# Kernel tuning notes

Hardware: AMD Instinct MI355X
Metric: run time of the kernel (lower is better)

The kernel has to match this reference:

```python
import jax, jax.numpy as jnp
import numpy as np

D_MODEL = 1024
N_HEADS = 16
D_V = D_MODEL // N_HEADS  # 64


def setup_inputs() -> dict:
    key = jax.random.key(0)
    k1, k2, k3, k4, k5, k6 = jax.random.split(key, 6)
    N, L = 2, 2048
    return {
        "queries": jax.random.normal(k1, (N, L, D_MODEL), jnp.float32),
        "keys": jax.random.normal(k2, (N, L, D_MODEL), jnp.float32),
        "values": jax.random.normal(k3, (N, L, D_MODEL), jnp.float32),
        # key-padding mask, 0 = masked out (broadcast over heads and queries)
        "mask": jax.random.randint(k4, (N, 1, 1, L), 0, 2).astype(jnp.int32),
        # torch nn.Linear(d_model, d_model): weight [out, in], bias [out]
        "fc_w": jax.random.normal(k5, (D_MODEL, D_MODEL), jnp.float32) / np.sqrt(D_MODEL).astype(np.float32),
        "fc_b": jax.random.normal(k6, (D_MODEL,), jnp.float32) * 0.01,
    }


def reference(queries, keys, values, mask, fc_w, fc_b):
    N, Lq, _ = queries.shape
    Lk = keys.shape[1]
    # NOTE: the source defines Q/K/V Linear layers but never applies them in forward.
    q = queries.reshape(N, Lq, N_HEADS, D_V).transpose(0, 2, 1, 3)  # [N,H,Lq,Dv]
    k = keys.reshape(N, Lk, N_HEADS, D_V)                            # [N,Lk,H,Dv]
    v = values.reshape(N, Lk, N_HEADS, D_V)                          # [N,Lk,H,Dv]
    energy = jnp.einsum('nhqd,nkhd->nhqk', q, k)                     # QK^T
    energy = jnp.where(mask == 0, -jnp.inf, energy)                  # masked_fill
    # faithful to source: scale by sqrt(d_model), applied after masking
    attn = jax.nn.softmax(energy / jnp.sqrt(jnp.float32(D_MODEL)), axis=-1)
    out = jnp.einsum('nhqk,nkhd->nqhd', attn, v).reshape(N, Lq, N_HEADS * D_V)
    return out @ fc_w.T + fc_b
```

## Files before the change

kernel.cpp:

```cpp
#include <hip/hip_runtime.h>
#include <hip/hip_bf16.h>

#define SEQL 2048
#define DMODEL 1024

typedef short bf16x8 __attribute__((ext_vector_type(8)));
typedef short bf16x4 __attribute__((ext_vector_type(4)));
typedef float f32x4 __attribute__((ext_vector_type(4)));
typedef unsigned short u16;

__device__ __forceinline__ u16 f2bf(float f) {
    union { float f; unsigned u; } v; v.f = f;
    unsigned r = v.u + 0x7FFFu + ((v.u >> 16) & 1u);
    return (u16)(r >> 16);
}

__device__ __forceinline__ float fexp2(float x) {
#if __has_builtin(__builtin_amdgcn_exp2f)
    return __builtin_amdgcn_exp2f(x);
#else
    return exp2f(x);
#endif
}

#define SCALE2 0.04508422f

__device__ __forceinline__ void async16(u16* lds, const u16* g) {
    __builtin_amdgcn_global_load_lds(
        (const __attribute__((address_space(1))) unsigned int*)g,
        (__attribute__((address_space(3))) unsigned int*)lds,
        16, 0, 0);
}


#define TSTR 72

__global__ __launch_bounds__(256) void pack_all(
    const float* __restrict__ kg, const float* __restrict__ wg,
    const float* __restrict__ vg, const int* __restrict__ mg,
    u16* __restrict__ kb, u16* __restrict__ wb, u16* __restrict__ vtb,
    float* __restrict__ maskf)
{
    __shared__ __align__(16) u16 T[64 * TSTR];
    const int b = blockIdx.x, t = threadIdx.x;
    u16 o[8];
    if (b < 2048) {
        const int e0 = (b * 256 + t) * 8;
        const int n = e0 >> 21;
        const int s = (e0 >> 10) & 2047;
        const int dm = e0 & 1023, h = dm >> 6, d0 = dm & 63;
        const float4 x0 = *(const float4*)(kg + e0);
        const float4 x1 = *(const float4*)(kg + e0 + 4);
        o[0]=f2bf(x0.x); o[1]=f2bf(x0.y); o[2]=f2bf(x0.z); o[3]=f2bf(x0.w);
        o[4]=f2bf(x1.x); o[5]=f2bf(x1.y); o[6]=f2bf(x1.z); o[7]=f2bf(x1.w);
        const int kt = s >> 6, st = (s >> 4) & 3, m = s & 15;
        const int f = d0 >> 5, qd = (d0 >> 3) & 3;
        u16* dst = kb + ((size_t)((n * 16 + h) * 32 + kt)) * 4096
                      + (st * 2 + f) * 512 + (m + 16 * qd) * 8;
        *(bf16x8*)dst = *(bf16x8*)o;
    } else if (b < 2560) {
        const int e0 = ((b - 2048) * 256 + t) * 8;
        const int col = e0 >> 10, k0 = e0 & 1023;
        const float4 x0 = *(const float4*)(wg + e0);
        const float4 x1 = *(const float4*)(wg + e0 + 4);
        o[0]=f2bf(x0.x); o[1]=f2bf(x0.y); o[2]=f2bf(x0.z); o[3]=f2bf(x0.w);
        o[4]=f2bf(x1.x); o[5]=f2bf(x1.y); o[6]=f2bf(x1.z); o[7]=f2bf(x1.w);
        const int cb = col >> 6, cj = (col >> 4) & 3, m = col & 15;
        const int kt = k0 >> 6, f = (k0 >> 5) & 1, qd = (k0 >> 3) & 3;
        u16* dst = wb + ((size_t)((cb * 16 + kt) * 8 + cj * 2 + f)) * 512
                      + (m + 16 * qd) * 8;
        *(bf16x8*)dst = *(bf16x8*)o;
    } else if (b < 3584) {
        const int bb = b - 2560;
        const int kt = bb & 31, h = (bb >> 5) & 15, n = bb >> 9;
        {
            const int s = t >> 2, d0 = (t & 3) * 16;
            const float* src = vg + ((size_t)(n * SEQL + kt * 64 + s) * DMODEL) + h * 64 + d0;
            u16 w16[16];
            #pragma unroll
            for (int j = 0; j < 16; ++j) w16[j] = f2bf(src[j]);
            *(bf16x8*)&T[s * TSTR + d0]     = *(bf16x8*)&w16[0];
            *(bf16x8*)&T[s * TSTR + d0 + 8] = *(bf16x8*)&w16[8];
        }
        __syncthreads();
        {
            const int d = t >> 2, k0 = (t & 3) * 16;
            u16 w16[16];
            #pragma unroll
            for (int j = 0; j < 16; ++j) w16[j] = T[(k0 + j) * TSTR + d];
            const int t4 = d >> 4, dr = d & 15;
            u16* base = vtb + ((size_t)((n * 16 + h) * 32 + kt)) * 4096;
            #pragma unroll
            for (int g = 0; g < 2; ++g) {
                const int key0 = k0 + g * 8;
                const int kk = key0 >> 5, qk = (key0 >> 3) & 3;
                *(bf16x8*)(base + (t4 * 2 + kk) * 512 + (dr + 16 * qk) * 8)
                    = *(bf16x8*)&w16[g * 8];
            }
        }
    } else {
        #pragma unroll
        for (int i = 0; i < 16; ++i) {
            const int idx = t * 16 + i;
            maskf[idx] = mg[idx] ? 0.0f : -1.0e5f;
        }
    }
}

#define OSPLIT 4194304
#define LSPLIT 65536

template<int NSPLIT>
__global__ __launch_bounds__(256) void attn_kernel(
    const float* __restrict__ qg, const u16* __restrict__ kb,
    const u16* __restrict__ vtb, const float* __restrict__ maskf,
    u16* __restrict__ xb, float* __restrict__ opart, float* __restrict__ lpart)
{
    __shared__ __align__(16) u16 SM[24576];
    u16* const K_lds = SM;
    u16* const V_lds = SM + 8192;
    u16* const P_lds = SM + 16384;

    const int blk = blockIdx.x;
    const int qblk = blk & 15;
    const int h = (blk >> 4) & 15;
    const int n = (blk >> 8) & 1;
    const int split = blk >> 9;
    const int tid = threadIdx.x;
    const int wave = tid >> 6, lane = tid & 63;
    const int lrow = lane & 15, quad = lane >> 4;
    const int q0 = qblk * 128;

    const u16* ksrc0 = kb  + ((size_t)(n * 16 + h)) * 131072;
    const u16* vsrc0 = vtb + ((size_t)(n * 16 + h)) * 131072;
    const float* mrow = maskf + n * SEQL;

    const int ktlo = split * (32 / NSPLIT);
    const int kthi = ktlo + (32 / NSPLIT);

    {
        const u16* ks = ksrc0 + (size_t)ktlo * 4096;
        const u16* vs = vsrc0 + (size_t)ktlo * 4096;
        #pragma unroll
        for (int i = 0; i < 2; ++i) {
            const int ch = tid + i * 256;
            async16(&K_lds[ch * 8], ks + ch * 8);
            async16(&V_lds[ch * 8], vs + ch * 8);
        }
    }

    bf16x8 qf[2][2];
    #pragma unroll
    for (int qi = 0; qi < 2; ++qi) {
        const float* qp = qg + ((size_t)(n * SEQL + q0 + wave * 32 + qi * 16 + lrow) * DMODEL) + h * 64 + quad * 8;
        #pragma unroll
        for (int f = 0; f < 2; ++f) {
            const float4 a = *(const float4*)(qp + f * 32);
            const float4 c = *(const float4*)(qp + f * 32 + 4);
            u16* dst = (u16*)&qf[qi][f];
            dst[0]=f2bf(a.x); dst[1]=f2bf(a.y); dst[2]=f2bf(a.z); dst[3]=f2bf(a.w);
            dst[4]=f2bf(c.x); dst[5]=f2bf(c.y); dst[6]=f2bf(c.z); dst[7]=f2bf(c.w);
        }
    }

    bf16x8 onesf;
    #pragma unroll
    for (int j = 0; j < 8; ++j) ((u16*)&onesf)[j] = 0x3F80;

    f32x4 oacc[2][4];
    f32x4 lacc[2];
    #pragma unroll
    for (int qi = 0; qi < 2; ++qi) {
        lacc[qi] = (f32x4){0.f, 0.f, 0.f, 0.f};
        #pragma unroll
        for (int t4 = 0; t4 < 4; ++t4) oacc[qi][t4] = (f32x4){0.f, 0.f, 0.f, 0.f};
    }

    __syncthreads();

    for (int kt = ktlo; kt < kthi; ++kt) {
        const int cur = (kt - ktlo) & 1;
        const u16* const Kc = K_lds + cur * 4096;
        const u16* const Vc = V_lds + cur * 4096;

        if (kt + 1 < kthi) {
            const int nxt = cur ^ 1;
            const u16* ks = ksrc0 + (size_t)(kt + 1) * 4096;
            const u16* vs = vsrc0 + (size_t)(kt + 1) * 4096;
            #pragma unroll
            for (int i = 0; i < 2; ++i) {
                const int ch = tid + i * 256;
                async16(&K_lds[nxt * 4096 + ch * 8], ks + ch * 8);
                async16(&V_lds[nxt * 4096 + ch * 8], vs + ch * 8);
            }
        }

        #pragma unroll
        for (int st = 0; st < 4; ++st) {
            const bf16x8 kf0 = *(const bf16x8*)&Kc[(st * 2 + 0) * 512 + lane * 8];
            const bf16x8 kf1 = *(const bf16x8*)&Kc[(st * 2 + 1) * 512 + lane * 8];
            const f32x4 mv = *(const f32x4*)&mrow[kt * 64 + st * 16 + quad * 4];
            const int kk = st >> 1;
            const int qk = (st & 1) * 2 + (quad >> 1);
            const int j0 = (quad & 1) * 4;
            #pragma unroll
            for (int qi = 0; qi < 2; ++qi) {
                f32x4 sa = (f32x4){0.f, 0.f, 0.f, 0.f};
                sa = __builtin_amdgcn_mfma_f32_16x16x32_bf16(kf0, qf[qi][0], sa, 0, 0, 0);
                sa = __builtin_amdgcn_mfma_f32_16x16x32_bf16(kf1, qf[qi][1], sa, 0, 0, 0);
                float e0v = fexp2(fmaf(sa[0], SCALE2, mv[0]));
                float e1v = fexp2(fmaf(sa[1], SCALE2, mv[1]));
                float e2v = fexp2(fmaf(sa[2], SCALE2, mv[2]));
                float e3v = fexp2(fmaf(sa[3], SCALE2, mv[3]));
                __hip_bfloat162 h0 = __float22bfloat162_rn(make_float2(e0v, e1v));
                __hip_bfloat162 h1 = __float22bfloat162_rn(make_float2(e2v, e3v));
                union { unsigned u[2]; bf16x4 v; } pk;
                pk.u[0] = *(unsigned*)&h0;
                pk.u[1] = *(unsigned*)&h1;
                *(bf16x4*)&P_lds[wave * 2048 + (qi * 2 + kk) * 512 + (lrow + 16 * qk) * 8 + j0] = pk.v;
            }
        }
        asm volatile("s_waitcnt lgkmcnt(0)" ::: "memory");

        bf16x8 vf[4][2];
        #pragma unroll
        for (int t4 = 0; t4 < 4; ++t4) {
            vf[t4][0] = *(const bf16x8*)&Vc[(t4 * 2 + 0) * 512 + lane * 8];
            vf[t4][1] = *(const bf16x8*)&Vc[(t4 * 2 + 1) * 512 + lane * 8];
        }
        #pragma unroll
        for (int qi = 0; qi < 2; ++qi) {
            const bf16x8 pf0 = *(const bf16x8*)&P_lds[wave * 2048 + (qi * 2 + 0) * 512 + lane * 8];
            const bf16x8 pf1 = *(const bf16x8*)&P_lds[wave * 2048 + (qi * 2 + 1) * 512 + lane * 8];
            lacc[qi] = __builtin_amdgcn_mfma_f32_16x16x32_bf16(pf0, onesf, lacc[qi], 0, 0, 0);
            lacc[qi] = __builtin_amdgcn_mfma_f32_16x16x32_bf16(pf1, onesf, lacc[qi], 0, 0, 0);
            #pragma unroll
            for (int t4 = 0; t4 < 4; ++t4) {
                oacc[qi][t4] = __builtin_amdgcn_mfma_f32_16x16x32_bf16(pf0, vf[t4][0], oacc[qi][t4], 0, 0, 0);
                oacc[qi][t4] = __builtin_amdgcn_mfma_f32_16x16x32_bf16(pf1, vf[t4][1], oacc[qi][t4], 0, 0, 0);
            }
        }

        __syncthreads();
    }

    if (NSPLIT == 1) {
        #pragma unroll
        for (int qi = 0; qi < 2; ++qi)
            #pragma unroll
            for (int r = 0; r < 4; ++r) {
                const float rinv = 1.0f / lacc[qi][r];
                const int row = n * SEQL + q0 + wave * 32 + qi * 16 + quad * 4 + r;
                const int rb = row >> 7, rt = (row >> 4) & 7, m = row & 15;
                #pragma unroll
                for (int t4 = 0; t4 < 4; ++t4) {
                    const int f = t4 >> 1;
                    const int qd = (t4 & 1) * 2 + (lrow >> 3);
                    xb[((size_t)((rb * 16 + h) * 16 + rt * 2 + f)) * 512
                       + (m + 16 * qd) * 8 + (lrow & 7)] = f2bf(oacc[qi][t4][r] * rinv);
                }
            }
    } else {
        #pragma unroll
        for (int qi = 0; qi < 2; ++qi) {
            #pragma unroll
            for (int r = 0; r < 4; ++r) {
                const int q = q0 + wave * 32 + qi * 16 + quad * 4 + r;
                float* op = opart + (size_t)split * OSPLIT + (size_t)(n * SEQL + q) * DMODEL + h * 64 + lrow;
                #pragma unroll
                for (int t4 = 0; t4 < 4; ++t4)
                    op[t4 * 16] = oacc[qi][t4][r];
                if (lrow == 0)
                    lpart[split * LSPLIT + (n * SEQL + q) * 16 + h] = lacc[qi][r];
            }
        }
    }
}

template<int NSPLIT>
__global__ __launch_bounds__(256) void reduce_norm(
    const float* __restrict__ opart, const float* __restrict__ lpart,
    u16* __restrict__ xb)
{
    const int gid = blockIdx.x * 256 + threadIdx.x;
    const int e0 = gid * 8;
    const int row = e0 >> 10, k0 = e0 & 1023, h = k0 >> 6;
    float lsum = 0.f;
    #pragma unroll
    for (int s = 0; s < NSPLIT; ++s) lsum += lpart[s * LSPLIT + row * 16 + h];
    const float rinv = 1.0f / lsum;
    float a[8] = {0.f,0.f,0.f,0.f,0.f,0.f,0.f,0.f};
    #pragma unroll
    for (int s = 0; s < NSPLIT; ++s) {
        const float4 x0 = *(const float4*)(opart + (size_t)s * OSPLIT + e0);
        const float4 x1 = *(const float4*)(opart + (size_t)s * OSPLIT + e0 + 4);
        a[0]+=x0.x; a[1]+=x0.y; a[2]+=x0.z; a[3]+=x0.w;
        a[4]+=x1.x; a[5]+=x1.y; a[6]+=x1.z; a[7]+=x1.w;
    }
    u16 o[8];
    #pragma unroll
    for (int j = 0; j < 8; ++j) o[j] = f2bf(a[j] * rinv);
    const int rb = row >> 7, rt = (row >> 4) & 7, m = row & 15;
    const int kt = k0 >> 6, f = (k0 >> 5) & 1, qd = (k0 >> 3) & 3;
    *(bf16x8*)(xb + ((size_t)((rb * 16 + kt) * 16 + rt * 2 + f)) * 512
                  + (m + 16 * qd) * 8) = *(bf16x8*)o;
}

__global__ __launch_bounds__(256) void fc_kernel(
    const u16* __restrict__ xb, const u16* __restrict__ wb,
    const float* __restrict__ bias, float* __restrict__ out)
{
    __shared__ __align__(16) u16 SM[24576];
    u16* const X_lds = SM;
    u16* const W_lds = SM + 16384;

    const int blk = blockIdx.x;
    const int cb = blk & 15, rb = blk >> 4;
    const int tid = threadIdx.x;
    const int wave = tid >> 6, lane = tid & 63;
    const int lrow = lane & 15, quad = lane >> 4;

    const u16* xs0 = xb + ((size_t)rb * 16) * 8192;
    const u16* ws0 = wb + ((size_t)cb * 16) * 4096;

    f32x4 acc[2][4];
    #pragma unroll
    for (int ri = 0; ri < 2; ++ri)
        #pragma unroll
        for (int cj = 0; cj < 4; ++cj) acc[ri][cj] = (f32x4){0.f, 0.f, 0.f, 0.f};

    {
        #pragma unroll
        for (int i = 0; i < 4; ++i) {
            const int ch = tid + i * 256;
            async16(&X_lds[ch * 8], xs0 + ch * 8);
        }
        #pragma unroll
        for (int i = 0; i < 2; ++i) {
            const int ch = tid + i * 256;
            async16(&W_lds[ch * 8], ws0 + ch * 8);
        }
    }
    __syncthreads();

    for (int kt = 0; kt < 16; ++kt) {
        const int cur = kt & 1;
        const u16* const Xc = X_lds + cur * 8192;
        const u16* const Wc = W_lds + cur * 4096;

        if (kt + 1 < 16) {
            const int nxt = cur ^ 1;
            const u16* xs = xs0 + (size_t)(kt + 1) * 8192;
            const u16* ws = ws0 + (size_t)(kt + 1) * 4096;
            #pragma unroll
            for (int i = 0; i < 4; ++i) {
                const int ch = tid + i * 256;
                async16(&X_lds[nxt * 8192 + ch * 8], xs + ch * 8);
            }
            #pragma unroll
            for (int i = 0; i < 2; ++i) {
                const int ch = tid + i * 256;
                async16(&W_lds[nxt * 4096 + ch * 8], ws + ch * 8);
            }
        }

        bf16x8 af[2][2];
        #pragma unroll
        for (int ri = 0; ri < 2; ++ri) {
            af[ri][0] = *(const bf16x8*)&Xc[((wave * 2 + ri) * 2 + 0) * 512 + lane * 8];
            af[ri][1] = *(const bf16x8*)&Xc[((wave * 2 + ri) * 2 + 1) * 512 + lane * 8];
        }
        #pragma unroll
        for (int cj = 0; cj < 4; ++cj) {
            const bf16x8 bf0 = *(const bf16x8*)&Wc[(cj * 2 + 0) * 512 + lane * 8];
            const bf16x8 bf1 = *(const bf16x8*)&Wc[(cj * 2 + 1) * 512 + lane * 8];
            #pragma unroll
            for (int ri = 0; ri < 2; ++ri) {
                acc[ri][cj] = __builtin_amdgcn_mfma_f32_16x16x32_bf16(af[ri][0], bf0, acc[ri][cj], 0, 0, 0);
                acc[ri][cj] = __builtin_amdgcn_mfma_f32_16x16x32_bf16(af[ri][1], bf1, acc[ri][cj], 0, 0, 0);
            }
        }

        __syncthreads();
    }

    const int row0 = rb * 128, col0 = cb * 64;
    #pragma unroll
    for (int ri = 0; ri < 2; ++ri)
        #pragma unroll
        for (int cj = 0; cj < 4; ++cj) {
            const int col = col0 + cj * 16 + lrow;
            const float bv = bias[col];
            #pragma unroll
            for (int r = 0; r < 4; ++r)
                out[(size_t)(row0 + wave * 32 + ri * 16 + quad * 4 + r) * DMODEL + col] = acc[ri][cj][r] + bv;
        }
}

extern "C" void kernel_launch(void* const* d_in, const int* in_sizes, int n_in,
                              void* d_out, int out_size, void* d_ws, size_t ws_size,
                              hipStream_t stream) {
    const float* q   = (const float*)d_in[0];
    const float* k   = (const float*)d_in[1];
    const float* v   = (const float*)d_in[2];
    const int*   m   = (const int*)d_in[3];
    const float* fcw = (const float*)d_in[4];
    const float* fcb = (const float*)d_in[5];
    float* out = (float*)d_out;

    char* ws = (char*)d_ws;
    u16*   kbuf  = (u16*)(ws);
    u16*   vtbuf = (u16*)(ws + (8u  << 20));
    u16*   wbuf  = (u16*)(ws + (16u << 20));
    u16*   xbuf  = (u16*)(ws + (18u << 20));
    float* maskf = (float*)(ws + (26u << 20));
    float* opart = (float*)(ws + (27u << 20));
    float* lpart = (float*)(ws + (59u << 20));
    const bool split2 = ws_size >= (60u << 20);

    pack_all<<<dim3(3585), dim3(256), 0, stream>>>(k, fcw, v, m, kbuf, wbuf, vtbuf, maskf);
    if (split2) {
        attn_kernel<2><<<dim3(1024), dim3(256), 0, stream>>>(q, kbuf, vtbuf, maskf, xbuf, opart, lpart);
        reduce_norm<2><<<dim3(2048), dim3(256), 0, stream>>>(opart, lpart, xbuf);
    } else {
        attn_kernel<1><<<dim3(512), dim3(256), 0, stream>>>(q, kbuf, vtbuf, maskf, xbuf, opart, lpart);
    }
    fc_kernel<<<dim3(512), dim3(256), 0, stream>>>(xbuf, wbuf, fcb, out);
}
```

Before: 182.1 us.

## Switch attention to 32x32x16 MFMA with register-resident P via permlane swaps

Rewrites the attention inner loop to use 32x32x16 bf16 MFMAs, computing S as K·Q so that the exponentiated probabilities can be rearranged in registers with v_permlane32_swap and fed straight into the PV MFMA. This removes the P round-trip through LDS and the extra ones-vector MFMAs used for row sums, which are now accumulated in VALU. The K and V^T packing layouts change to match the new fragment shapes, and s_setprio is added around the MFMA bursts. The cost is higher register pressure from 16-wide accumulators and a dependence on the permlane32 swap instruction being available on this target.

```diff
diff --git a/kernel.cpp b/kernel.cpp
--- a/kernel.cpp
+++ b/kernel.cpp
@@ -7,6 +7,7 @@
 typedef short bf16x8 __attribute__((ext_vector_type(8)));
 typedef short bf16x4 __attribute__((ext_vector_type(4)));
 typedef float f32x4 __attribute__((ext_vector_type(4)));
+typedef float f32x16 __attribute__((ext_vector_type(16)));
 typedef unsigned short u16;
 
 __device__ __forceinline__ u16 f2bf(float f) {
@@ -24,6 +25,15 @@
 }
 
 #define SCALE2 0.04508422f
+
+__device__ __forceinline__ unsigned pkbf(float lo, float hi_) {
+    __hip_bfloat162 hh = __float22bfloat162_rn(make_float2(lo, hi_));
+    return *(unsigned*)&hh;
+}
+
+__device__ __forceinline__ void plswap(unsigned &a, unsigned &b) {
+    asm volatile("v_permlane32_swap_b32 %0, %1" : "+v"(a), "+v"(b));
+}
 
 __device__ __forceinline__ void async16(u16* lds, const u16* g) {
     __builtin_amdgcn_global_load_lds(
@@ -53,10 +63,10 @@
         const float4 x1 = *(const float4*)(kg + e0 + 4);
         o[0]=f2bf(x0.x); o[1]=f2bf(x0.y); o[2]=f2bf(x0.z); o[3]=f2bf(x0.w);
         o[4]=f2bf(x1.x); o[5]=f2bf(x1.y); o[6]=f2bf(x1.z); o[7]=f2bf(x1.w);
-        const int kt = s >> 6, st = (s >> 4) & 3, m = s & 15;
-        const int f = d0 >> 5, qd = (d0 >> 3) & 3;
+        const int kt = s >> 6, key = s & 63, kh = key >> 5, m = key & 31;
+        const int f = d0 >> 4, h2 = (d0 >> 3) & 1;
         u16* dst = kb + ((size_t)((n * 16 + h) * 32 + kt)) * 4096
-                      + (st * 2 + f) * 512 + (m + 16 * qd) * 8;
+                      + (kh * 4 + f) * 512 + (m + 32 * h2) * 8;
         *(bf16x8*)dst = *(bf16x8*)o;
     } else if (b < 2560) {
         const int e0 = ((b - 2048) * 256 + t) * 8;
@@ -88,15 +98,12 @@
             u16 w16[16];
             #pragma unroll
             for (int j = 0; j < 16; ++j) w16[j] = T[(k0 + j) * TSTR + d];
-            const int t4 = d >> 4, dr = d & 15;
-            u16* base = vtb + ((size_t)((n * 16 + h) * 32 + kt)) * 4096;
-            #pragma unroll
-            for (int g = 0; g < 2; ++g) {
-                const int key0 = k0 + g * 8;
-                const int kk = key0 >> 5, qk = (key0 >> 3) & 3;
-                *(bf16x8*)(base + (t4 * 2 + kk) * 512 + (dr + 16 * qk) * 8)
-                    = *(bf16x8*)&w16[g * 8];
-            }
+            const int kgp = t & 3;
+            const int dh = d >> 5, m = d & 31;
+            u16* base = vtb + ((size_t)((n * 16 + h) * 32 + kt)) * 4096
+                            + (kgp * 2 + dh) * 512;
+            *(bf16x8*)(base + m * 8)        = *(bf16x8*)&w16[0];
+            *(bf16x8*)(base + (m + 32) * 8) = *(bf16x8*)&w16[8];
         }
     } else {
         #pragma unroll
@@ -116,10 +123,10 @@
     const u16* __restrict__ vtb, const float* __restrict__ maskf,
     u16* __restrict__ xb, float* __restrict__ opart, float* __restrict__ lpart)
 {
-    __shared__ __align__(16) u16 SM[24576];
+    __shared__ __align__(16) u16 SM[16640];
     u16* const K_lds = SM;
     u16* const V_lds = SM + 8192;
-    u16* const P_lds = SM + 16384;
+    float* const LS  = (float*)(SM + 16384);
 
     const int blk = blockIdx.x;
     const int qblk = blk & 15;
@@ -128,7 +135,7 @@
     const int split = blk >> 9;
     const int tid = threadIdx.x;
     const int wave = tid >> 6, lane = tid & 63;
-    const int lrow = lane & 15, quad = lane >> 4;
+    const int l31 = lane & 31, hi = lane >> 5;
     const int q0 = qblk * 128;
 
     const u16* ksrc0 = kb  + ((size_t)(n * 16 + h)) * 131072;
@@ -149,32 +156,26 @@
         }
     }
 
-    bf16x8 qf[2][2];
-    #pragma unroll
-    for (int qi = 0; qi < 2; ++qi) {
-        const float* qp = qg + ((size_t)(n * SEQL + q0 + wave * 32 + qi * 16 + lrow) * DMODEL) + h * 64 + quad * 8;
-        #pragma unroll
-        for (int f = 0; f < 2; ++f) {
-            const float4 a = *(const float4*)(qp + f * 32);
-            const float4 c = *(const float4*)(qp + f * 32 + 4);
-            u16* dst = (u16*)&qf[qi][f];
+    bf16x8 qf[4];
+    {
+        const float* qp = qg + ((size_t)(n * SEQL + q0 + wave * 32 + l31) * DMODEL)
+                        + h * 64 + hi * 8;
+        #pragma unroll
+        for (int f = 0; f < 4; ++f) {
+            const float4 a = *(const float4*)(qp + f * 16);
+            const float4 c = *(const float4*)(qp + f * 16 + 4);
+            u16* dst = (u16*)&qf[f];
             dst[0]=f2bf(a.x); dst[1]=f2bf(a.y); dst[2]=f2bf(a.z); dst[3]=f2bf(a.w);
             dst[4]=f2bf(c.x); dst[5]=f2bf(c.y); dst[6]=f2bf(c.z); dst[7]=f2bf(c.w);
         }
     }
 
-    bf16x8 onesf;
-    #pragma unroll
-    for (int j = 0; j < 8; ++j) ((u16*)&onesf)[j] = 0x3F80;
-
-    f32x4 oacc[2][4];
-    f32x4 lacc[2];
-    #pragma unroll
-    for (int qi = 0; qi < 2; ++qi) {
-        lacc[qi] = (f32x4){0.f, 0.f, 0.f, 0.f};
-        #pragma unroll
-        for (int t4 = 0; t4 < 4; ++t4) oacc[qi][t4] = (f32x4){0.f, 0.f, 0.f, 0.f};
-    }
+    f32x16 oacc[2];
+    #pragma unroll
+    for (int dh = 0; dh < 2; ++dh)
+        #pragma unroll
+        for (int i = 0; i < 16; ++i) oacc[dh][i] = 0.f;
+    float lsum = 0.f;
 
     __syncthreads();
 
@@ -196,84 +197,110 @@
         }
 
         #pragma unroll
-        for (int st = 0; st < 4; ++st) {
-            const bf16x8 kf0 = *(const bf16x8*)&Kc[(st * 2 + 0) * 512 + lane * 8];
-            const bf16x8 kf1 = *(const bf16x8*)&Kc[(st * 2 + 1) * 512 + lane * 8];
-            const f32x4 mv = *(const f32x4*)&mrow[kt * 64 + st * 16 + quad * 4];
-            const int kk = st >> 1;
-            const int qk = (st & 1) * 2 + (quad >> 1);
-            const int j0 = (quad & 1) * 4;
-            #pragma unroll
-            for (int qi = 0; qi < 2; ++qi) {
-                f32x4 sa = (f32x4){0.f, 0.f, 0.f, 0.f};
-                sa = __builtin_amdgcn_mfma_f32_16x16x32_bf16(kf0, qf[qi][0], sa, 0, 0, 0);
-                sa = __builtin_amdgcn_mfma_f32_16x16x32_bf16(kf1, qf[qi][1], sa, 0, 0, 0);
-                float e0v = fexp2(fmaf(sa[0], SCALE2, mv[0]));
-                float e1v = fexp2(fmaf(sa[1], SCALE2, mv[1]));
-                float e2v = fexp2(fmaf(sa[2], SCALE2, mv[2]));
-                float e3v = fexp2(fmaf(sa[3], SCALE2, mv[3]));
-                __hip_bfloat162 h0 = __float22bfloat162_rn(make_float2(e0v, e1v));
-                __hip_bfloat162 h1 = __float22bfloat162_rn(make_float2(e2v, e3v));
-                union { unsigned u[2]; bf16x4 v; } pk;
-                pk.u[0] = *(unsigned*)&h0;
-                pk.u[1] = *(unsigned*)&h1;
-                *(bf16x4*)&P_lds[wave * 2048 + (qi * 2 + kk) * 512 + (lrow + 16 * qk) * 8 + j0] = pk.v;
-            }
-        }
-        asm volatile("s_waitcnt lgkmcnt(0)" ::: "memory");
-
-        bf16x8 vf[4][2];
-        #pragma unroll
-        for (int t4 = 0; t4 < 4; ++t4) {
-            vf[t4][0] = *(const bf16x8*)&Vc[(t4 * 2 + 0) * 512 + lane * 8];
-            vf[t4][1] = *(const bf16x8*)&Vc[(t4 * 2 + 1) * 512 + lane * 8];
-        }
-        #pragma unroll
-        for (int qi = 0; qi < 2; ++qi) {
-            const bf16x8 pf0 = *(const bf16x8*)&P_lds[wave * 2048 + (qi * 2 + 0) * 512 + lane * 8];
-            const bf16x8 pf1 = *(const bf16x8*)&P_lds[wave * 2048 + (qi * 2 + 1) * 512 + lane * 8];
-            lacc[qi] = __builtin_amdgcn_mfma_f32_16x16x32_bf16(pf0, onesf, lacc[qi], 0, 0, 0);
-            lacc[qi] = __builtin_amdgcn_mfma_f32_16x16x32_bf16(pf1, onesf, lacc[qi], 0, 0, 0);
-            #pragma unroll
-            for (int t4 = 0; t4 < 4; ++t4) {
-                oacc[qi][t4] = __builtin_amdgcn_mfma_f32_16x16x32_bf16(pf0, vf[t4][0], oacc[qi][t4], 0, 0, 0);
-                oacc[qi][t4] = __builtin_amdgcn_mfma_f32_16x16x32_bf16(pf1, vf[t4][1], oacc[qi][t4], 0, 0, 0);
+        for (int kh = 0; kh < 2; ++kh) {
+            const bf16x8 kf0 = *(const bf16x8*)&Kc[(kh * 4 + 0) * 512 + lane * 8];
+            const bf16x8 kf1 = *(const bf16x8*)&Kc[(kh * 4 + 1) * 512 + lane * 8];
+            const bf16x8 kf2 = *(const bf16x8*)&Kc[(kh * 4 + 2) * 512 + lane * 8];
+            const bf16x8 kf3 = *(const bf16x8*)&Kc[(kh * 4 + 3) * 512 + lane * 8];
+            f32x16 sacc;
+            #pragma unroll
+            for (int i = 0; i < 16; ++i) sacc[i] = 0.f;
+            __builtin_amdgcn_s_setprio(1);
+            sacc = __builtin_amdgcn_mfma_f32_32x32x16_bf16(kf0, qf[0], sacc, 0, 0, 0);
+            sacc = __builtin_amdgcn_mfma_f32_32x32x16_bf16(kf1, qf[1], sacc, 0, 0, 0);
+            sacc = __builtin_amdgcn_mfma_f32_32x32x16_bf16(kf2, qf[2], sacc, 0, 0, 0);
+            sacc = __builtin_amdgcn_mfma_f32_32x32x16_bf16(kf3, qf[3], sacc, 0, 0, 0);
+            __builtin_amdgcn_s_setprio(0);
+
+            const float* mp = mrow + kt * 64 + kh * 32 + 4 * hi;
+            const f32x4 m0 = *(const f32x4*)(mp);
+            const f32x4 m1 = *(const f32x4*)(mp + 8);
+            const f32x4 m2 = *(const f32x4*)(mp + 16);
+            const f32x4 m3 = *(const f32x4*)(mp + 24);
+            float e[16];
+            #pragma unroll
+            for (int r = 0; r < 4; ++r) {
+                e[r]      = fexp2(fmaf(sacc[r],      SCALE2, m0[r]));
+                e[4 + r]  = fexp2(fmaf(sacc[4 + r],  SCALE2, m1[r]));
+                e[8 + r]  = fexp2(fmaf(sacc[8 + r],  SCALE2, m2[r]));
+                e[12 + r] = fexp2(fmaf(sacc[12 + r], SCALE2, m3[r]));
+            }
+            lsum += ((e[0]+e[1])+(e[2]+e[3])) + ((e[4]+e[5])+(e[6]+e[7]))
+                  + ((e[8]+e[9])+(e[10]+e[11])) + ((e[12]+e[13])+(e[14]+e[15]));
+
+            unsigned w0 = pkbf(e[0],  e[1]),  w1 = pkbf(e[2],  e[3]);
+            unsigned w2 = pkbf(e[4],  e[5]),  w3 = pkbf(e[6],  e[7]);
+            unsigned w4 = pkbf(e[8],  e[9]),  w5 = pkbf(e[10], e[11]);
+            unsigned w6 = pkbf(e[12], e[13]), w7 = pkbf(e[14], e[15]);
+
+            plswap(w0, w2);
+            plswap(w1, w3);
+            union { unsigned u[4]; bf16x8 v; } A0;
+            A0.u[0] = w0; A0.u[1] = w1; A0.u[2] = w2; A0.u[3] = w3;
+            {
+                const int kg = kh * 2 + 0;
+                const bf16x8 vf0 = *(const bf16x8*)&Vc[(kg * 2 + 0) * 512 + lane * 8];
+                const bf16x8 vf1 = *(const bf16x8*)&Vc[(kg * 2 + 1) * 512 + lane * 8];
+                __builtin_amdgcn_s_setprio(1);
+                oacc[0] = __builtin_amdgcn_mfma_f32_32x32x16_bf16(A0.v, vf0, oacc[0], 0, 0, 0);
+                oacc[1] = __builtin_amdgcn_mfma_f32_32x32x16_bf16(A0.v, vf1, oacc[1], 0, 0, 0);
+                __builtin_amdgcn_s_setprio(0);
+            }
+            plswap(w4, w6);
+            plswap(w5, w7);
+            union { unsigned u[4]; bf16x8 v; } A1;
+            A1.u[0] = w4; A1.u[1] = w5; A1.u[2] = w6; A1.u[3] = w7;
+            {
+                const int kg = kh * 2 + 1;
+                const bf16x8 vf2 = *(const bf16x8*)&Vc[(kg * 2 + 0) * 512 + lane * 8];
+                const bf16x8 vf3 = *(const bf16x8*)&Vc[(kg * 2 + 1) * 512 + lane * 8];
+                __builtin_amdgcn_s_setprio(1);
+                oacc[0] = __builtin_amdgcn_mfma_f32_32x32x16_bf16(A1.v, vf2, oacc[0], 0, 0, 0);
+                oacc[1] = __builtin_amdgcn_mfma_f32_32x32x16_bf16(A1.v, vf3, oacc[1], 0, 0, 0);
+                __builtin_amdgcn_s_setprio(0);
             }
         }
 
         __syncthreads();
     }
 
+    const float s_full = lsum + __shfl_xor(lsum, 32);
+
     if (NSPLIT == 1) {
-        #pragma unroll
-        for (int qi = 0; qi < 2; ++qi)
-            #pragma unroll
-            for (int r = 0; r < 4; ++r) {
-                const float rinv = 1.0f / lacc[qi][r];
-                const int row = n * SEQL + q0 + wave * 32 + qi * 16 + quad * 4 + r;
-                const int rb = row >> 7, rt = (row >> 4) & 7, m = row & 15;
+        if (lane < 32) LS[wave * 32 + l31] = s_full;
+        __syncthreads();
+        f32x4 rv[4];
+        #pragma unroll
+        for (int g = 0; g < 4; ++g)
+            rv[g] = *(const f32x4*)&LS[wave * 32 + g * 8 + 4 * hi];
+        #pragma unroll
+        for (int dh = 0; dh < 2; ++dh) {
+            const int c = l31;
+            #pragma unroll
+            for (int g = 0; g < 4; ++g)
                 #pragma unroll
-                for (int t4 = 0; t4 < 4; ++t4) {
-                    const int f = t4 >> 1;
-                    const int qd = (t4 & 1) * 2 + (lrow >> 3);
-                    xb[((size_t)((rb * 16 + h) * 16 + rt * 2 + f)) * 512
-                       + (m + 16 * qd) * 8 + (lrow & 7)] = f2bf(oacc[qi][t4][r] * rinv);
+                for (int r = 0; r < 4; ++r) {
+                    const int row = n * SEQL + q0 + wave * 32 + g * 8 + 4 * hi + r;
+                    const int rb = row >> 7, rt = (row >> 4) & 7, m = row & 15;
+                    xb[((size_t)((rb * 16 + h) * 16 + rt * 2 + dh)) * 512
+                       + (m + 16 * ((c >> 3) & 3)) * 8 + (c & 7)]
+                        = f2bf(oacc[dh][g * 4 + r] / rv[g][r]);
                 }
-            }
+        }
     } else {
         #pragma unroll
-        for (int qi = 0; qi < 2; ++qi) {
-            #pragma unroll
-            for (int r = 0; r < 4; ++r) {
-                const int q = q0 + wave * 32 + qi * 16 + quad * 4 + r;
-                float* op = opart + (size_t)split * OSPLIT + (size_t)(n * SEQL + q) * DMODEL + h * 64 + lrow;
+        for (int dh = 0; dh < 2; ++dh) {
+            #pragma unroll
+            for (int g = 0; g < 4; ++g)
                 #pragma unroll
-                for (int t4 = 0; t4 < 4; ++t4)
-                    op[t4 * 16] = oacc[qi][t4][r];
-                if (lrow == 0)
-                    lpart[split * LSPLIT + (n * SEQL + q) * 16 + h] = lacc[qi][r];
-            }
-        }
+                for (int r = 0; r < 4; ++r) {
+                    const int q = q0 + wave * 32 + g * 8 + 4 * hi + r;
+                    opart[(size_t)split * OSPLIT + (size_t)(n * SEQL + q) * DMODEL
+                          + h * 64 + dh * 32 + l31] = oacc[dh][g * 4 + r];
+                }
+        }
+        if (lane < 32)
+            lpart[split * LSPLIT + (n * SEQL + q0 + wave * 32 + l31) * 16 + h] = s_full;
     }
 }
 
```

Result: slower. 187.6 us (+3.0%).

## Fuse split-K attention and reduction into one 512-thread block

Applied to the files above, without the earlier changes.

Replaces the two-way key-split attention kernel plus its separate reduce/normalize kernel with a single kernel. Each 512-thread block runs two halves of 4 waves, one per key half, and combines their partial outputs and row sums through shared memory before normalizing and writing bf16. This removes the global partial buffers and one kernel launch. In exchange the double-buffered async K/V prefetch becomes single-buffered with two barriers per tile, so load latency is no longer overlapped with compute.

```diff
diff --git a/kernel.cpp b/kernel.cpp
--- a/kernel.cpp
+++ b/kernel.cpp
@@ -107,52 +107,36 @@
     }
 }
 
-#define OSPLIT 4194304
-#define LSPLIT 65536
-
-template<int NSPLIT>
-__global__ __launch_bounds__(256) void attn_kernel(
+__global__ __launch_bounds__(512) void attn_fused(
     const float* __restrict__ qg, const u16* __restrict__ kb,
     const u16* __restrict__ vtb, const float* __restrict__ maskf,
-    u16* __restrict__ xb, float* __restrict__ opart, float* __restrict__ lpart)
+    u16* __restrict__ xb)
 {
-    __shared__ __align__(16) u16 SM[24576];
-    u16* const K_lds = SM;
-    u16* const V_lds = SM + 8192;
-    u16* const P_lds = SM + 16384;
+    __shared__ __align__(16) u16 SM[32768];
 
     const int blk = blockIdx.x;
     const int qblk = blk & 15;
     const int h = (blk >> 4) & 15;
-    const int n = (blk >> 8) & 1;
-    const int split = blk >> 9;
+    const int n = blk >> 8;
     const int tid = threadIdx.x;
     const int wave = tid >> 6, lane = tid & 63;
+    const int half = wave >> 2, w4 = wave & 3;
+    const int tloc = tid & 255;
     const int lrow = lane & 15, quad = lane >> 4;
     const int q0 = qblk * 128;
 
-    const u16* ksrc0 = kb  + ((size_t)(n * 16 + h)) * 131072;
-    const u16* vsrc0 = vtb + ((size_t)(n * 16 + h)) * 131072;
-    const float* mrow = maskf + n * SEQL;
-
-    const int ktlo = split * (32 / NSPLIT);
-    const int kthi = ktlo + (32 / NSPLIT);
-
-    {
-        const u16* ks = ksrc0 + (size_t)ktlo * 4096;
-        const u16* vs = vsrc0 + (size_t)ktlo * 4096;
-        #pragma unroll
-        for (int i = 0; i < 2; ++i) {
-            const int ch = tid + i * 256;
-            async16(&K_lds[ch * 8], ks + ch * 8);
-            async16(&V_lds[ch * 8], vs + ch * 8);
-        }
-    }
+    u16* const K_lds = SM + half * 4096;
+    u16* const V_lds = SM + 8192 + half * 4096;
+    u16* const P_lds = SM + 16384 + wave * 2048;
+
+    const u16* ksrc = kb  + ((size_t)(n * 16 + h)) * 131072 + (size_t)half * 65536;
+    const u16* vsrc = vtb + ((size_t)(n * 16 + h)) * 131072 + (size_t)half * 65536;
+    const float* mrow = maskf + n * SEQL + half * 1024;
 
     bf16x8 qf[2][2];
     #pragma unroll
     for (int qi = 0; qi < 2; ++qi) {
-        const float* qp = qg + ((size_t)(n * SEQL + q0 + wave * 32 + qi * 16 + lrow) * DMODEL) + h * 64 + quad * 8;
+        const float* qp = qg + ((size_t)(n * SEQL + q0 + w4 * 32 + qi * 16 + lrow) * DMODEL) + h * 64 + quad * 8;
         #pragma unroll
         for (int f = 0; f < 2; ++f) {
             const float4 a = *(const float4*)(qp + f * 32);
@@ -176,30 +160,25 @@
         for (int t4 = 0; t4 < 4; ++t4) oacc[qi][t4] = (f32x4){0.f, 0.f, 0.f, 0.f};
     }
 
-    __syncthreads();
-
-    for (int kt = ktlo; kt < kthi; ++kt) {
-        const int cur = (kt - ktlo) & 1;
-        const u16* const Kc = K_lds + cur * 4096;
-        const u16* const Vc = V_lds + cur * 4096;
-
-        if (kt + 1 < kthi) {
-            const int nxt = cur ^ 1;
-            const u16* ks = ksrc0 + (size_t)(kt + 1) * 4096;
-            const u16* vs = vsrc0 + (size_t)(kt + 1) * 4096;
-            #pragma unroll
-            for (int i = 0; i < 2; ++i) {
-                const int ch = tid + i * 256;
-                async16(&K_lds[nxt * 4096 + ch * 8], ks + ch * 8);
-                async16(&V_lds[nxt * 4096 + ch * 8], vs + ch * 8);
-            }
-        }
+    for (int i = 0; i < 16; ++i) {
+        __syncthreads();
+        {
+            const u16* ks = ksrc + (size_t)i * 4096;
+            const u16* vs = vsrc + (size_t)i * 4096;
+            #pragma unroll
+            for (int c = 0; c < 2; ++c) {
+                const int ch = tloc + c * 256;
+                async16(&K_lds[ch * 8], ks + ch * 8);
+                async16(&V_lds[ch * 8], vs + ch * 8);
+            }
+        }
+        __syncthreads();
 
         #pragma unroll
         for (int st = 0; st < 4; ++st) {
-            const bf16x8 kf0 = *(const bf16x8*)&Kc[(st * 2 + 0) * 512 + lane * 8];
-            const bf16x8 kf1 = *(const bf16x8*)&Kc[(st * 2 + 1) * 512 + lane * 8];
-            const f32x4 mv = *(const f32x4*)&mrow[kt * 64 + st * 16 + quad * 4];
+            const bf16x8 kf0 = *(const bf16x8*)&K_lds[(st * 2 + 0) * 512 + lane * 8];
+            const bf16x8 kf1 = *(const bf16x8*)&K_lds[(st * 2 + 1) * 512 + lane * 8];
+            const f32x4 mv = *(const f32x4*)&mrow[i * 64 + st * 16 + quad * 4];
             const int kk = st >> 1;
             const int qk = (st & 1) * 2 + (quad >> 1);
             const int j0 = (quad & 1) * 4;
@@ -217,7 +196,7 @@
                 union { unsigned u[2]; bf16x4 v; } pk;
                 pk.u[0] = *(unsigned*)&h0;
                 pk.u[1] = *(unsigned*)&h1;
-                *(bf16x4*)&P_lds[wave * 2048 + (qi * 2 + kk) * 512 + (lrow + 16 * qk) * 8 + j0] = pk.v;
+                *(bf16x4*)&P_lds[(qi * 2 + kk) * 512 + (lrow + 16 * qk) * 8 + j0] = pk.v;
             }
         }
         asm volatile("s_waitcnt lgkmcnt(0)" ::: "memory");
@@ -225,13 +204,13 @@
         bf16x8 vf[4][2];
         #pragma unroll
         for (int t4 = 0; t4 < 4; ++t4) {
-            vf[t4][0] = *(const bf16x8*)&Vc[(t4 * 2 + 0) * 512 + lane * 8];
-            vf[t4][1] = *(const bf16x8*)&Vc[(t4 * 2 + 1) * 512 + lane * 8];
+            vf[t4][0] = *(const bf16x8*)&V_lds[(t4 * 2 + 0) * 512 + lane * 8];
+            vf[t4][1] = *(const bf16x8*)&V_lds[(t4 * 2 + 1) * 512 + lane * 8];
         }
         #pragma unroll
         for (int qi = 0; qi < 2; ++qi) {
-            const bf16x8 pf0 = *(const bf16x8*)&P_lds[wave * 2048 + (qi * 2 + 0) * 512 + lane * 8];
-            const bf16x8 pf1 = *(const bf16x8*)&P_lds[wave * 2048 + (qi * 2 + 1) * 512 + lane * 8];
+            const bf16x8 pf0 = *(const bf16x8*)&P_lds[(qi * 2 + 0) * 512 + lane * 8];
+            const bf16x8 pf1 = *(const bf16x8*)&P_lds[(qi * 2 + 1) * 512 + lane * 8];
             lacc[qi] = __builtin_amdgcn_mfma_f32_16x16x32_bf16(pf0, onesf, lacc[qi], 0, 0, 0);
             lacc[qi] = __builtin_amdgcn_mfma_f32_16x16x32_bf16(pf1, onesf, lacc[qi], 0, 0, 0);
             #pragma unroll
@@ -240,17 +219,39 @@
                 oacc[qi][t4] = __builtin_amdgcn_mfma_f32_16x16x32_bf16(pf1, vf[t4][1], oacc[qi][t4], 0, 0, 0);
             }
         }
-
-        __syncthreads();
-    }
-
-    if (NSPLIT == 1) {
+    }
+
+    __syncthreads();
+    float* const Pf = (float*)(SM + 16384);
+    float* const Lf = (float*)SM;
+    if (half) {
+        float* dst = Pf + (size_t)(w4 * 64 + lane) * 32;
+        float* ld  = Lf + (size_t)(w4 * 64 + lane) * 8;
+        #pragma unroll
+        for (int qi = 0; qi < 2; ++qi) {
+            *(f32x4*)(ld + qi * 4) = lacc[qi];
+            #pragma unroll
+            for (int t4 = 0; t4 < 4; ++t4)
+                *(f32x4*)(dst + qi * 16 + t4 * 4) = oacc[qi][t4];
+        }
+    }
+    __syncthreads();
+    if (!half) {
+        const float* src = Pf + (size_t)(w4 * 64 + lane) * 32;
+        const float* ls  = Lf + (size_t)(w4 * 64 + lane) * 8;
+        #pragma unroll
+        for (int qi = 0; qi < 2; ++qi) {
+            lacc[qi] += *(const f32x4*)(ls + qi * 4);
+            #pragma unroll
+            for (int t4 = 0; t4 < 4; ++t4)
+                oacc[qi][t4] += *(const f32x4*)(src + qi * 16 + t4 * 4);
+        }
         #pragma unroll
         for (int qi = 0; qi < 2; ++qi)
             #pragma unroll
             for (int r = 0; r < 4; ++r) {
                 const float rinv = 1.0f / lacc[qi][r];
-                const int row = n * SEQL + q0 + wave * 32 + qi * 16 + quad * 4 + r;
+                const int row = n * SEQL + q0 + w4 * 32 + qi * 16 + quad * 4 + r;
                 const int rb = row >> 7, rt = (row >> 4) & 7, m = row & 15;
                 #pragma unroll
                 for (int t4 = 0; t4 < 4; ++t4) {
@@ -260,50 +261,7 @@
                        + (m + 16 * qd) * 8 + (lrow & 7)] = f2bf(oacc[qi][t4][r] * rinv);
                 }
             }
-    } else {
-        #pragma unroll
-        for (int qi = 0; qi < 2; ++qi) {
-            #pragma unroll
-            for (int r = 0; r < 4; ++r) {
-                const int q = q0 + wave * 32 + qi * 16 + quad * 4 + r;
-                float* op = opart + (size_t)split * OSPLIT + (size_t)(n * SEQL + q) * DMODEL + h * 64 + lrow;
-                #pragma unroll
-                for (int t4 = 0; t4 < 4; ++t4)
-                    op[t4 * 16] = oacc[qi][t4][r];
-                if (lrow == 0)
-                    lpart[split * LSPLIT + (n * SEQL + q) * 16 + h] = lacc[qi][r];
-            }
-        }
-    }
-}
-
-template<int NSPLIT>
-__global__ __launch_bounds__(256) void reduce_norm(
-    const float* __restrict__ opart, const float* __restrict__ lpart,
-    u16* __restrict__ xb)
-{
-    const int gid = blockIdx.x * 256 + threadIdx.x;
-    const int e0 = gid * 8;
-    const int row = e0 >> 10, k0 = e0 & 1023, h = k0 >> 6;
-    float lsum = 0.f;
-    #pragma unroll
-    for (int s = 0; s < NSPLIT; ++s) lsum += lpart[s * LSPLIT + row * 16 + h];
-    const float rinv = 1.0f / lsum;
-    float a[8] = {0.f,0.f,0.f,0.f,0.f,0.f,0.f,0.f};
-    #pragma unroll
-    for (int s = 0; s < NSPLIT; ++s) {
-        const float4 x0 = *(const float4*)(opart + (size_t)s * OSPLIT + e0);
-        const float4 x1 = *(const float4*)(opart + (size_t)s * OSPLIT + e0 + 4);
-        a[0]+=x0.x; a[1]+=x0.y; a[2]+=x0.z; a[3]+=x0.w;
-        a[4]+=x1.x; a[5]+=x1.y; a[6]+=x1.z; a[7]+=x1.w;
-    }
-    u16 o[8];
-    #pragma unroll
-    for (int j = 0; j < 8; ++j) o[j] = f2bf(a[j] * rinv);
-    const int rb = row >> 7, rt = (row >> 4) & 7, m = row & 15;
-    const int kt = k0 >> 6, f = (k0 >> 5) & 1, qd = (k0 >> 3) & 3;
-    *(bf16x8*)(xb + ((size_t)((rb * 16 + kt) * 16 + rt * 2 + f)) * 512
-                  + (m + 16 * qd) * 8) = *(bf16x8*)o;
+    }
 }
 
 __global__ __launch_bounds__(256) void fc_kernel(
@@ -414,16 +372,8 @@
     u16*   wbuf  = (u16*)(ws + (16u << 20));
     u16*   xbuf  = (u16*)(ws + (18u << 20));
     float* maskf = (float*)(ws + (26u << 20));
-    float* opart = (float*)(ws + (27u << 20));
-    float* lpart = (float*)(ws + (59u << 20));
-    const bool split2 = ws_size >= (60u << 20);
 
     pack_all<<<dim3(3585), dim3(256), 0, stream>>>(k, fcw, v, m, kbuf, wbuf, vtbuf, maskf);
-    if (split2) {
-        attn_kernel<2><<<dim3(1024), dim3(256), 0, stream>>>(q, kbuf, vtbuf, maskf, xbuf, opart, lpart);
-        reduce_norm<2><<<dim3(2048), dim3(256), 0, stream>>>(opart, lpart, xbuf);
-    } else {
-        attn_kernel<1><<<dim3(512), dim3(256), 0, stream>>>(q, kbuf, vtbuf, maskf, xbuf, opart, lpart);
-    }
+    attn_fused<<<dim3(512), dim3(512), 0, stream>>>(q, kbuf, vtbuf, maskf, xbuf);
     fc_kernel<<<dim3(512), dim3(256), 0, stream>>>(xbuf, wbuf, fcb, out);
 }
```

New measurement: 171.4 us. 1.06x faster.
